# Kernel tuning notes

Hardware: AMD Instinct MI355X
Metric: run time of the kernel (lower is better)

## Reference

```python
import jax, jax.numpy as jnp
import numpy as np

BATCH, D_IN, D_OUT = 2048, 1024, 4096


def setup_inputs() -> dict:
    key = jax.random.key(0)
    kx, kw = jax.random.split(key)
    x = jax.random.normal(kx, (BATCH, D_IN), dtype=jnp.float32)
    W = jax.random.normal(kw, (D_IN, D_OUT), dtype=jnp.float32)  # nn.Parameter init: N(0,1)
    return {"x": x, "W": W}


def reference(x, W):
    # out[b,o] = -1/2 * sum_i (x[b,i] - W[i,o])^2
    # instead of materializing the [B, O, I] broadcast tensor.
    x_sq = jnp.sum(x * x, axis=1, keepdims=True)          # [B, 1]
    w_sq = jnp.sum(W * W, axis=0, keepdims=True)          # [1, O]
    xw = jnp.matmul(x, W)                                  # [B, O] GEMM
    return -0.5 * (x_sq - 2.0 * xw + w_sq)
```

## Files before the change

kernel.cpp:

```cpp
#include <hip/hip_runtime.h>
#include <stdint.h>

#define BATCH 2048
#define DIN   1024
#define DOUT  4096


__device__ __forceinline__ ushort f2bf(float f) {
    uint32_t u = __float_as_uint(f);
    u += 0x7fffu + ((u >> 16) & 1u);
    return (ushort)(u >> 16);
}

__device__ __forceinline__ void async_copy16(const void* gsrc, void* ldst) {
    __builtin_amdgcn_global_load_lds(
        reinterpret_cast<uint32_t __attribute__((address_space(1)))*>(
            reinterpret_cast<uintptr_t>(gsrc)),
        reinterpret_cast<uint32_t __attribute__((address_space(3)))*>(
            reinterpret_cast<uintptr_t>(ldst)),
        16, 0, 0);
}

typedef __bf16 bf16x8 __attribute__((ext_vector_type(8)));
typedef float  f32x4  __attribute__((ext_vector_type(4)));


__global__ __launch_bounds__(256) void prep_x(const float* __restrict__ x,
                                              ushort* __restrict__ xb,
                                              float* __restrict__ xsq) {
    const int row = blockIdx.x;
    const int t = threadIdx.x;
    const float4 v = *(const float4*)(x + (size_t)row * DIN + t * 4);
    ushort4 pk;
    pk.x = f2bf(v.x); pk.y = f2bf(v.y); pk.z = f2bf(v.z); pk.w = f2bf(v.w);
    *(ushort4*)(xb + (size_t)row * DIN + t * 4) = pk;

    float s = v.x * v.x + v.y * v.y + v.z * v.z + v.w * v.w;
    #pragma unroll
    for (int off = 32; off > 0; off >>= 1) s += __shfl_down(s, off);
    __shared__ float ws[4];
    if ((t & 63) == 0) ws[t >> 6] = s;
    __syncthreads();
    if (t == 0) xsq[row] = ws[0] + ws[1] + ws[2] + ws[3];
}

__global__ __launch_bounds__(256) void prep_w(const float* __restrict__ W,
                                              ushort* __restrict__ wbt,
                                              float* __restrict__ wsq) {
    __shared__ float tile[64][65];
    const int o0 = blockIdx.x * 64;
    const int i0 = blockIdx.y * 64;
    const int tx = threadIdx.x & 63;
    const int ty = threadIdx.x >> 6;

    float ssq = 0.f;
    #pragma unroll
    for (int r = ty; r < 64; r += 4) {
        const float v = W[(size_t)(i0 + r) * DOUT + o0 + tx];
        tile[r][tx] = v;
        ssq += v * v;
    }
    atomicAdd(&wsq[o0 + tx], ssq);
    __syncthreads();
    #pragma unroll
    for (int r = ty; r < 64; r += 4) {
        const float v = tile[tx][r];
        wbt[(size_t)(o0 + r) * DIN + i0 + tx] = f2bf(v);
    }
}

#define BM 128
#define BN 128
#define BK 32

__global__ __launch_bounds__(256, 2) void gemm_bt_epi(
    const ushort* __restrict__ A,
    const ushort* __restrict__ Bt,
    const float* __restrict__ xsq,
    const float* __restrict__ wsq,
    float* __restrict__ out) {
    __shared__ __align__(16) ushort sA[BM * BK];
    __shared__ __align__(16) ushort sB[BN * BK];

    const int tid  = threadIdx.x;
    const int wv   = tid >> 6;
    const int lane = tid & 63;
    const int wr = wv >> 1, wc = wv & 1;
    const int m0 = blockIdx.y * BM;
    const int n0 = blockIdx.x * BN;

    const int st_row = wv * 32 + (lane >> 2);
    const int st_col = (lane & 3) * 8;

    const ushort* agp0 = A  + (size_t)(m0 + st_row)      * DIN + st_col;
    const ushort* agp1 = A  + (size_t)(m0 + st_row + 16) * DIN + st_col;
    const ushort* bgp0 = Bt + (size_t)(n0 + st_row)      * DIN + st_col;
    const ushort* bgp1 = Bt + (size_t)(n0 + st_row + 16) * DIN + st_col;

    ushort* sA0 = &sA[wv * 1024];
    ushort* sA1 = &sA[wv * 1024 + 512];
    ushort* sB0 = &sB[wv * 1024];
    ushort* sB1 = &sB[wv * 1024 + 512];

    f32x4 acc[4][4] = {};

    const int a_row = wr * 64 + (lane & 15);
    const int b_row = wc * 64 + (lane & 15);
    const int kq    = (lane >> 4) * 8;

    for (int kt = 0; kt < DIN; kt += BK) {
        __syncthreads();
        async_copy16(agp0 + kt, sA0);
        async_copy16(agp1 + kt, sA1);
        async_copy16(bgp0 + kt, sB0);
        async_copy16(bgp1 + kt, sB1);
        __syncthreads();

        bf16x8 fa[4], fb[4];
        #pragma unroll
        for (int i = 0; i < 4; ++i)
            fa[i] = *(const bf16x8*)&sA[(a_row + i * 16) * BK + kq];
        #pragma unroll
        for (int i = 0; i < 4; ++i)
            fb[i] = *(const bf16x8*)&sB[(b_row + i * 16) * BK + kq];

        #pragma unroll
        for (int mi = 0; mi < 4; ++mi)
            #pragma unroll
            for (int ni = 0; ni < 4; ++ni)
                acc[mi][ni] = __builtin_amdgcn_mfma_f32_16x16x32_bf16(
                    fa[mi], fb[ni], acc[mi][ni], 0, 0, 0);
    }

    const int er = (lane >> 4) * 4;
    const int ec = lane & 15;
    #pragma unroll
    for (int mi = 0; mi < 4; ++mi) {
        const int row = m0 + wr * 64 + mi * 16 + er;
        #pragma unroll
        for (int ni = 0; ni < 4; ++ni) {
            const int col = n0 + wc * 64 + ni * 16 + ec;
            const float wterm = wsq[col];
            #pragma unroll
            for (int r = 0; r < 4; ++r) {
                out[(size_t)(row + r) * DOUT + col] =
                    acc[mi][ni][r] - 0.5f * (xsq[row + r] + wterm);
            }
        }
    }
}


extern "C" void kernel_launch(void* const* d_in, const int* in_sizes, int n_in,
                              void* d_out, int out_size, void* d_ws, size_t ws_size,
                              hipStream_t stream) {
    const float* x = (const float*)d_in[0];
    const float* W = (const float*)d_in[1];
    float* out = (float*)d_out;

    char* ws = (char*)d_ws;
    ushort* xb  = (ushort*)ws;
    ushort* wbt = (ushort*)(ws + (4u << 20));
    float*  xsq = (float*)(ws + (12u << 20));
    float*  wsq = (float*)(ws + (12u << 20) + (16u << 10));

    hipMemsetAsync(wsq, 0, DOUT * sizeof(float), stream);
    prep_x<<<BATCH, 256, 0, stream>>>(x, xb, xsq);
    prep_w<<<dim3(DOUT / 64, DIN / 64), 256, 0, stream>>>(W, wbt, wsq);
    gemm_bt_epi<<<dim3(DOUT / BN, BATCH / BM), 256, 0, stream>>>(xb, wbt, xsq, wsq, out);
}
```

Measured before the change: 110.1 us.

## Double-buffer GEMM LDS tiles with BK=64 and XOR swizzle; vectorize W prep

The GEMM now uses two LDS buffers with BK doubled to 64, so the next tile's async global-to-LDS copy is issued before computing on the current one, and there is one barrier per iteration instead of two. LDS rows are XOR-swizzled in 8-element chunks to cut bank conflicts on fragment reads. prep_w switches to float4 loads and ushort4 stores and reduces column sums in shared memory before a single global atomic per column. The cost is more LDS per block (64KB), which may limit occupancy at 2 blocks per CU.

```diff
diff --git a/kernel.cpp b/kernel.cpp
--- a/kernel.cpp
+++ b/kernel.cpp
@@ -48,30 +48,49 @@
                                               ushort* __restrict__ wbt,
                                               float* __restrict__ wsq) {
     __shared__ float tile[64][65];
+    __shared__ float csum[64];
     const int o0 = blockIdx.x * 64;
     const int i0 = blockIdx.y * 64;
-    const int tx = threadIdx.x & 63;
-    const int ty = threadIdx.x >> 6;
-
-    float ssq = 0.f;
-    #pragma unroll
-    for (int r = ty; r < 64; r += 4) {
-        const float v = W[(size_t)(i0 + r) * DOUT + o0 + tx];
-        tile[r][tx] = v;
-        ssq += v * v;
-    }
-    atomicAdd(&wsq[o0 + tx], ssq);
-    __syncthreads();
-    #pragma unroll
-    for (int r = ty; r < 64; r += 4) {
-        const float v = tile[tx][r];
-        wbt[(size_t)(o0 + r) * DIN + i0 + tx] = f2bf(v);
+    const int t  = threadIdx.x;
+    const int c4 = (t & 15) * 4;
+    const int r0 = t >> 4;
+
+    if (t < 64) csum[t] = 0.f;
+    __syncthreads();
+
+    float ss0 = 0.f, ss1 = 0.f, ss2 = 0.f, ss3 = 0.f;
+    #pragma unroll
+    for (int p = 0; p < 4; ++p) {
+        const int r = r0 + p * 16;
+        const float4 v = *(const float4*)&W[(size_t)(i0 + r) * DOUT + o0 + c4];
+        tile[r][c4 + 0] = v.x; tile[r][c4 + 1] = v.y;
+        tile[r][c4 + 2] = v.z; tile[r][c4 + 3] = v.w;
+        ss0 += v.x * v.x; ss1 += v.y * v.y;
+        ss2 += v.z * v.z; ss3 += v.w * v.w;
+    }
+    atomicAdd(&csum[c4 + 0], ss0);
+    atomicAdd(&csum[c4 + 1], ss1);
+    atomicAdd(&csum[c4 + 2], ss2);
+    atomicAdd(&csum[c4 + 3], ss3);
+    __syncthreads();
+    if (t < 64) atomicAdd(&wsq[o0 + t], csum[t]);
+
+    #pragma unroll
+    for (int p = 0; p < 4; ++p) {
+        const int orow = r0 + p * 16;
+        ushort4 pk;
+        pk.x = f2bf(tile[c4 + 0][orow]);
+        pk.y = f2bf(tile[c4 + 1][orow]);
+        pk.z = f2bf(tile[c4 + 2][orow]);
+        pk.w = f2bf(tile[c4 + 3][orow]);
+        *(ushort4*)&wbt[(size_t)(o0 + orow) * DIN + i0 + c4] = pk;
     }
 }
 
 #define BM 128
 #define BN 128
-#define BK 32
+#define BK 64
+#define NT (DIN / BK)
 
 __global__ __launch_bounds__(256, 2) void gemm_bt_epi(
     const ushort* __restrict__ A,
@@ -79,8 +98,8 @@
     const float* __restrict__ xsq,
     const float* __restrict__ wsq,
     float* __restrict__ out) {
-    __shared__ __align__(16) ushort sA[BM * BK];
-    __shared__ __align__(16) ushort sB[BN * BK];
+    __shared__ __align__(16) ushort sA[2][BM * BK];
+    __shared__ __align__(16) ushort sB[2][BN * BK];
 
     const int tid  = threadIdx.x;
     const int wv   = tid >> 6;
@@ -89,47 +108,60 @@
     const int m0 = blockIdx.y * BM;
     const int n0 = blockIdx.x * BN;
 
-    const int st_row = wv * 32 + (lane >> 2);
-    const int st_col = (lane & 3) * 8;
-
-    const ushort* agp0 = A  + (size_t)(m0 + st_row)      * DIN + st_col;
-    const ushort* agp1 = A  + (size_t)(m0 + st_row + 16) * DIN + st_col;
-    const ushort* bgp0 = Bt + (size_t)(n0 + st_row)      * DIN + st_col;
-    const ushort* bgp1 = Bt + (size_t)(n0 + st_row + 16) * DIN + st_col;
-
-    ushort* sA0 = &sA[wv * 1024];
-    ushort* sA1 = &sA[wv * 1024 + 512];
-    ushort* sB0 = &sB[wv * 1024];
-    ushort* sB1 = &sB[wv * 1024 + 512];
+    const int srow = tid >> 3;
+    const int scol = (((tid & 7) ^ (srow & 7)) << 3);
+    const ushort* ag = A  + (size_t)(m0 + srow) * DIN + scol;
+    const ushort* bg = Bt + (size_t)(n0 + srow) * DIN + scol;
+
+    const int fr  = lane & 15;
+    const int q4  = lane >> 4;
+    const int x7  = lane & 7;
+    const int arow = wr * 64 + fr;
+    const int brow = wc * 64 + fr;
+    const int sl0 = ((q4)     ^ x7) << 3;
+    const int sl1 = ((4 + q4) ^ x7) << 3;
 
     f32x4 acc[4][4] = {};
 
-    const int a_row = wr * 64 + (lane & 15);
-    const int b_row = wc * 64 + (lane & 15);
-    const int kq    = (lane >> 4) * 8;
-
-    for (int kt = 0; kt < DIN; kt += BK) {
+    auto stage = [&](int b, int kt) {
+        ushort* da = &sA[b][0] + wv * 512;
+        ushort* db = &sB[b][0] + wv * 512;
+        #pragma unroll
+        for (int q = 0; q < 4; ++q) {
+            async_copy16(ag + (size_t)q * 32 * DIN + kt, da + q * 2048);
+            async_copy16(bg + (size_t)q * 32 * DIN + kt, db + q * 2048);
+        }
+    };
+
+    stage(0, 0);
+    __syncthreads();
+    int cur = 0;
+
+    for (int t = 0; t < NT; ++t) {
+        if (t + 1 < NT) stage(cur ^ 1, (t + 1) * BK);
+
+        const ushort* pa = &sA[cur][0];
+        const ushort* pb = &sB[cur][0];
+        bf16x8 fa[2][4], fb[2][4];
+        #pragma unroll
+        for (int i = 0; i < 4; ++i) {
+            fa[0][i] = *(const bf16x8*)&pa[(arow + i * 16) * BK + sl0];
+            fa[1][i] = *(const bf16x8*)&pa[(arow + i * 16) * BK + sl1];
+            fb[0][i] = *(const bf16x8*)&pb[(brow + i * 16) * BK + sl0];
+            fb[1][i] = *(const bf16x8*)&pb[(brow + i * 16) * BK + sl1];
+        }
+
+        #pragma unroll
+        for (int ks = 0; ks < 2; ++ks)
+            #pragma unroll
+            for (int mi = 0; mi < 4; ++mi)
+                #pragma unroll
+                for (int ni = 0; ni < 4; ++ni)
+                    acc[mi][ni] = __builtin_amdgcn_mfma_f32_16x16x32_bf16(
+                        fa[ks][mi], fb[ks][ni], acc[mi][ni], 0, 0, 0);
+
         __syncthreads();
-        async_copy16(agp0 + kt, sA0);
-        async_copy16(agp1 + kt, sA1);
-        async_copy16(bgp0 + kt, sB0);
-        async_copy16(bgp1 + kt, sB1);
-        __syncthreads();
-
-        bf16x8 fa[4], fb[4];
-        #pragma unroll
-        for (int i = 0; i < 4; ++i)
-            fa[i] = *(const bf16x8*)&sA[(a_row + i * 16) * BK + kq];
-        #pragma unroll
-        for (int i = 0; i < 4; ++i)
-            fb[i] = *(const bf16x8*)&sB[(b_row + i * 16) * BK + kq];
-
-        #pragma unroll
-        for (int mi = 0; mi < 4; ++mi)
-            #pragma unroll
-            for (int ni = 0; ni < 4; ++ni)
-                acc[mi][ni] = __builtin_amdgcn_mfma_f32_16x16x32_bf16(
-                    fa[mi], fb[ni], acc[mi][ni], 0, 0, 0);
+        cur ^= 1;
     }
 
     const int er = (lane >> 4) * 4;
```

After: 104.9 us (median of 2 runs). 4.7% less time.
